# Optimization experiments

Hardware: AMD Instinct MI355X
Metric: run time of the kernel (lower is better)

## Reference

```python
import jax, jax.numpy as jnp
import numpy as np

F_FRAMES = 8
N_BOXES = 1024
N_CLASSES = 8
LINKAGE_T = 0.2
IOU_T = 0.2
MAX_SEQS = 48  # fixed cap on number of extracted sequences (jit-friendly)
NEG = -1e9


def _iou_mat(a, b):
    # a: [N,4], b: [M,4] (xyxy) -> [N,M] pairwise IoU
    area_a = (a[:, 2] - a[:, 0]) * (a[:, 3] - a[:, 1])
    area_b = (b[:, 2] - b[:, 0]) * (b[:, 3] - b[:, 1])
    lt = jnp.maximum(a[:, None, :2], b[None, :, :2])
    rb = jnp.minimum(a[:, None, 2:], b[None, :, 2:])
    wh = jnp.clip(rb - lt, 0.0)
    inter = wh[..., 0] * wh[..., 1]
    return inter / (area_a[:, None] + area_b[None, :] - inter + 1e-8)


def _iou_vec(box, boxes):
    # box: [4], boxes: [N,4] -> [N]
    area_a = (box[2] - box[0]) * (box[3] - box[1])
    area_b = (boxes[:, 2] - boxes[:, 0]) * (boxes[:, 3] - boxes[:, 1])
    lt = jnp.maximum(box[:2], boxes[:, :2])
    rb = jnp.minimum(box[2:], boxes[:, 2:])
    wh = jnp.clip(rb - lt, 0.0)
    inter = wh[:, 0] * wh[:, 1]
    return inter / (area_a + area_b - inter + 1e-8)


def setup_inputs():
    key = jax.random.key(0)
    k1, k2, k3 = jax.random.split(key, 3)
    raw = jax.random.uniform(k1, (F_FRAMES, N_BOXES, 4), dtype=jnp.float32)
    cxy = raw[..., :2] * 100.0          # centers in a 100x100 image
    wh = raw[..., 2:] * 10.0 + 1.0      # sizes in [1, 11] so IoU links fire
    boxes = jnp.concatenate([cxy - 0.5 * wh, cxy + 0.5 * wh], axis=-1)
    scores = jax.random.uniform(k2, (F_FRAMES, N_BOXES), dtype=jnp.float32)
    classes = jax.random.randint(k3, (F_FRAMES, N_BOXES), 0, N_CLASSES, dtype=jnp.int32)
    return {"boxes": boxes, "scores": scores, "classes": classes}


def _seq_nms(boxes, scores, classes):
    F, N, _ = boxes.shape
    idxN = jnp.arange(N)
    # linkage graph between adjacent frames: IoU >= linkage_threshold and same class
    iou_cross = jax.vmap(_iou_mat)(boxes[:-1], boxes[1:])               # [F-1,N,N]
    adj = (iou_cross >= LINKAGE_T) & (classes[:-1, :, None] == classes[1:, None, :])
    adj_pad = jnp.concatenate([adj, jnp.zeros((1, N, N), bool)], 0)     # [F,N,N]

    def body(state, _):
        active, out_scores, done = state
        s = jnp.where(active, scores, 0.0)
        # DP backward over frames: best sequence score starting at each box
        ms_last = jnp.where(active[-1], s[-1], NEG)
        def dp_step(ms_next, xs):
            adj_f, act_f, act_n, s_f = xs
            eff = adj_f & act_f[:, None] & act_n[None, :]
            best_succ = jnp.max(jnp.where(eff, ms_next[None, :], 0.0), axis=1)
            ms_f = jnp.where(act_f, s_f + best_succ, NEG)
            return ms_f, ms_f
        xs = (adj[::-1], active[:-1][::-1], active[1:][::-1], s[:-1][::-1])
        _, ms_rev = jax.lax.scan(dp_step, ms_last, xs)
        ms = jnp.concatenate([ms_rev[::-1], ms_last[None]], 0)          # [F,N]
        flat = jnp.argmax(ms)
        fstar = (flat // N).astype(jnp.int32)
        istar = (flat % N).astype(jnp.int32)
        best_val = ms.reshape(-1)[flat]
        # trace the best sequence forward through the graph
        ms_next_pad = jnp.concatenate([ms[1:], jnp.full((1, N), NEG)], 0)
        act_next_pad = jnp.concatenate([active[1:], jnp.zeros((1, N), bool)], 0)
        def trace_step(carry, xs2):
            cur, in_seq = carry
            f, adj_f, ms_n, act_n = xs2
            start = (f == fstar)
            in_seq = in_seq | start
            cur = jnp.where(start, istar, cur)
            onehot = in_seq & (idxN == cur)
            row = adj_f[cur] & act_n
            has_link = jnp.any(row)
            nxt = jnp.argmax(jnp.where(row, ms_n, NEG)).astype(cur.dtype)
            cont = in_seq & has_link
            return (jnp.where(cont, nxt, cur), cont), onehot
        carry0 = (jnp.zeros((), jnp.int32), jnp.zeros((), bool))
        _, seq_mask = jax.lax.scan(
            trace_step, carry0,
            (jnp.arange(F, dtype=jnp.int32), adj_pad, ms_next_pad, act_next_pad))
        seq_len = jnp.sum(seq_mask)
        valid = (seq_len > 1) & (best_val > 0) & (~done)
        # rescore: average of the sequence's (original) scores over all its members
        avg = jnp.sum(jnp.where(seq_mask, scores, 0.0)) / jnp.maximum(seq_len, 1)
        out_scores = jnp.where(seq_mask & valid, avg, out_scores)
        # suppress same-class boxes overlapping the sequence box in each sequence frame
        seq_boxes = jnp.einsum('fn,fnd->fd', seq_mask.astype(boxes.dtype), boxes)
        frame_in = jnp.any(seq_mask, axis=1)
        cls_seq = jnp.sum(jnp.where(seq_mask, classes, 0), axis=1)
        iou_same = jax.vmap(_iou_vec)(seq_boxes, boxes)                 # [F,N]
        sup = frame_in[:, None] & (iou_same >= IOU_T) & (classes == cls_seq[:, None])
        active = active & ~(sup & valid)
        done = done | ~((seq_len > 1) & (best_val > 0))
        return (active, out_scores, done), None

    init = (jnp.ones((F, N), bool), scores, jnp.zeros((), bool))
    (active, out_scores, done), _ = jax.lax.scan(body, init, None, length=MAX_SEQS)
    return out_scores


def reference(boxes, scores, classes):
    return _seq_nms(boxes, scores, classes)
```

## Files before the change

kernel.cpp:

```cpp
#include <hip/hip_runtime.h>

typedef unsigned int u32;
typedef unsigned short u16;
typedef unsigned char u8;

#define NFR 8
#define NBX 1024
#define NTOT 8192
#define NROW 7168
#define MAXS 48
#define NEGV -1000000000.0f
#define OVTOT 256
#define OVPF 36
#define PSTRIDE 64
#define DEG_RECOMP 0xFFFF
#define ENC_RESCAN  ((3u << 30) | (1023u << 10) | 1023u)

#define WS_POOL 7168
#define WS_OVL  (7168 + 8192)
#define WS_OST2 (WS_OVL + 128)
#define WS_WORDS (WS_OST2 + 8)

__device__ __forceinline__ bool iou_ge(const float4 a, const float4 b) {
    float wx = __fsub_rn(fminf(a.z, b.z), fmaxf(a.x, b.x));
    if (!(wx > 0.0f)) return false;
    float wy = __fsub_rn(fminf(a.w, b.w), fmaxf(a.y, b.y));
    if (!(wy > 0.0f)) return false;
    float inter = __fmul_rn(wx, wy);
    float aa = __fmul_rn(__fsub_rn(a.z, a.x), __fsub_rn(a.w, a.y));
    float ab = __fmul_rn(__fsub_rn(b.z, b.x), __fsub_rn(b.w, b.y));
    float den = __fadd_rn(__fsub_rn(__fadd_rn(aa, ab), inter), 1e-8f);
    return __fdiv_rn(inter, den) >= 0.2f;
}

__device__ __forceinline__ int xbin(float x) {
    int b = (int)floorf(__fmul_rn(__fadd_rn(x, 6.0f), 0.2857142857f));
    return b < 0 ? 0 : (b > 31 ? 31 : b);
}


__global__ __launch_bounds__(1024) void seqnms_setup(const float4* __restrict__ gbox,
                                                     const int* __restrict__ classes,
                                                     u32* __restrict__ ws) {
    __shared__ u32 clsb[3][32];
    __shared__ u32 cmask[8][32];
    __shared__ u32 xbm[32][32];
    __shared__ u16 ovl_l[OVPF];
    __shared__ u32 ofill;

    const int f = blockIdx.x;
    const int t = threadIdx.x, gw = t >> 6, ln = t & 63;

    if (t < 32 * 32) ((u32*)xbm)[t] = 0;
    if (t < 256) ((u32*)cmask)[t] = 0;
    if (t < 96) ((u32*)clsb)[t] = 0;
    if (t == 0) ofill = 0;

    const float4 a4 = gbox[f * NBX + t];
    const int ca = classes[f * NBX + t];
    const float4 nb4 = gbox[(f + 1) * NBX + t];
    const int ncl = classes[(f + 1) * NBX + t];
    __syncthreads();

    {
        const u32 bit = 1u << (t & 31); const int wrd = t >> 5;
        int b0 = xbin(nb4.x), b1 = xbin(nb4.z);
        for (int b = b0; b <= b1; ++b) atomicOr(&xbm[wrd][b], bit);
        atomicOr(&cmask[ncl][wrd], bit);
        if (ncl & 1) atomicOr(&clsb[0][wrd], bit);
        if (ncl & 2) atomicOr(&clsb[1][wrd], bit);
        if (ncl & 4) atomicOr(&clsb[2][wrd], bit);
    }
    __syncthreads();

    {
        const int rb0 = xbin(a4.x), rb1 = xbin(a4.z);
        const float4* nb = gbox + (f + 1) * NBX;
        u32 cnt = 0, j0 = 0, j1 = 0, j2 = 0;
        for (int w = 0; w < 32; ++w) {
            u32 mx = xbm[w][rb0];
            for (int b = rb0 + 1; b <= rb1; ++b) mx |= xbm[w][b];
            if (!mx) continue;
            u32 m = mx & cmask[ca][w];
            while (m) {
                int b = __ffs(m) - 1;
                m &= m - 1;
                int j = w * 32 + b;
                if (iou_ge(a4, nb[j])) {
                    if (cnt == 0) j0 = j; else if (cnt == 1) j1 = j; else if (cnt == 2) j2 = j;
                    ++cnt;
                }
            }
        }
        u32 enc;
        if (cnt <= 3) enc = (cnt << 30) | (j2 << 20) | (j1 << 10) | j0;
        else {
            u32 sl = atomicAdd(&ofill, 1u);
            if (sl < OVPF) {
                u32 slot = (u32)(f * OVPF) + sl;
                ovl_l[sl] = (u16)t;
                ((u16*)(ws + WS_OVL))[slot] = (u16)t;
                enc = (3u << 30) | (slot << 10) | slot;
            } else enc = ENC_RESCAN;
        }
        ws[f * NBX + t] = enc;
    }
    __syncthreads();

    {
        u16* poolg = (u16*)(ws + WS_POOL);
        int cntc = (int)ofill; if (cntc > OVPF) cntc = OVPF;
        for (int sl = gw; sl < cntc; sl += 16) {
            int i = ovl_l[sl];
            int slot = f * OVPF + sl;
            int cai = classes[f * NBX + i];
            float4 ai = gbox[f * NBX + i];
            u32 mym = 0;
            if (ln < 32) {
                u32 m = ((cai & 1) ? clsb[0][ln] : ~clsb[0][ln])
                      & ((cai & 2) ? clsb[1][ln] : ~clsb[1][ln])
                      & ((cai & 4) ? clsb[2][ln] : ~clsb[2][ln]);
                while (m) {
                    int b = __ffs(m) - 1;
                    m &= m - 1;
                    if (iou_ge(ai, gbox[(f + 1) * NBX + ln * 32 + b])) mym |= 1u << b;
                }
            }
            int c = __popc(mym), inc = c;
            for (int off = 1; off < 64; off <<= 1) {
                int v = __shfl_up(inc, off);
                if (ln >= off) inc += v;
            }
            int deg = __shfl(inc, 63);
            int base = inc - c;
            if (deg <= PSTRIDE - 1) {
                if (ln == 0) poolg[slot * PSTRIDE] = (u16)deg;
                if (ln < 32) {
                    u32 m = mym; int idx = base;
                    while (m) {
                        int b = __ffs(m) - 1;
                        m &= m - 1;
                        poolg[slot * PSTRIDE + 1 + idx++] = (u16)(ln * 32 + b);
                    }
                }
            } else if (ln == 0) poolg[slot * PSTRIDE] = (u16)DEG_RECOMP;
        }
        if (t == 0) ws[WS_OST2 + f] = (u32)cntc;
    }
}

__global__ __launch_bounds__(512) void seqnms_iter(const float4* __restrict__ gbox,
                                                   const float* __restrict__ scores,
                                                   const int* __restrict__ classes,
                                                   float* __restrict__ out,
                                                   const u32* __restrict__ ws) {
    __shared__ float4 ms4[NTOT / 4];
    __shared__ float4 seqbox[NFR];
    __shared__ float ssc[NTOT];
    __shared__ u32 csr[NROW];
    __shared__ u32 clsb7[7][3][32];
    __shared__ u16 pool[OVTOT * PSTRIDE];
    __shared__ u8 cls8[NTOT];
    __shared__ u32 cnt_sh[8];
    __shared__ float redv[8];
    __shared__ int   redi[8];
    __shared__ int   sel_sh[NFR];
    __shared__ int   seqcls[NFR];
    __shared__ float avg_sh;
    __shared__ int   valid_sh, done_sh;
    __shared__ u16 ovl[OVTOT];
    __shared__ u8  ovact[OVTOT];

    float* ms = (float*)ms4;
    const int t = threadIdx.x, gw = t >> 6, ln = t & 63;
    const int sg = (gw << 3) + (ln >> 3), sl = ln & 7;

    for (int idx = t; idx < NROW; idx += 512) csr[idx] = ws[idx];
    u32* p32 = (u32*)pool;
    for (int idx = t; idx < OVTOT * PSTRIDE / 2; idx += 512) p32[idx] = ws[WS_POOL + idx];
    if (t < 128) ((u32*)ovl)[t] = ws[WS_OVL + t];
    if (t < 7) cnt_sh[t] = ws[WS_OST2 + t];
    if (t < OVTOT) ovact[t] = 1;
    if (t == 0) done_sh = 0;

    float psc2[2][NFR]; u32 pclp[2] = {0u, 0u};
    #pragma unroll
    for (int f = 0; f < NFR; ++f) {
        #pragma unroll
        for (int c = 0; c < 2; ++c) {
            int i = t + (c << 9);
            float s = scores[f * NBX + i];
            int cl = classes[f * NBX + i];
            psc2[c][f] = s;
            pclp[c] |= (u32)cl << (3 * f);
            out[f * NBX + i] = s;
            ssc[f * NBX + i] = s;
            cls8[f * NBX + i] = (u8)cl;
        }
    }
    if (t < 224) {
        int fr = (t >> 5) + 1, w = t & 31;
        u32 p0 = 0, p1 = 0, p2 = 0;
        for (int b = 0; b < 32; ++b) {
            int c = classes[fr * NBX + w * 32 + b];
            p0 |= (u32)(c & 1) << b;
            p1 |= (u32)((c >> 1) & 1) << b;
            p2 |= (u32)((c >> 2) & 1) << b;
        }
        clsb7[fr - 1][0][w] = p0; clsb7[fr - 1][1][w] = p1; clsb7[fr - 1][2][w] = p2;
    }
    __syncthreads();

    u32 pc2[2][7]; u32 lmask = 0;
    #pragma unroll
    for (int c = 0; c < 2; ++c) {
        #pragma unroll
        for (int f = 0; f < 7; ++f) {
            u32 p = csr[f * NBX + t + (c << 9)];
            pc2[c][f] = p;
            if ((p >> 30) == 3u && (p & 1023) == ((p >> 10) & 1023) && (p & 1023) != 1023)
                lmask |= 1u << (8 * c + f);
        }
    }
    int ose[7];
    #pragma unroll
    for (int f = 0; f < 7; ++f) {
        int cv = (int)cnt_sh[f]; if (cv > OVPF) cv = OVPF;
        ose[f] = __builtin_amdgcn_readfirstlane(f * OVPF + cv);
    }
    u32 act = 0xFFFFu;
    float ms7_0 = psc2[0][7], ms7_1 = psc2[1][7];
    ms[7 * NBX + t] = ms7_0;
    ms[7 * NBX + t + 512] = ms7_1;
    __syncthreads();

    for (int it = 0; it < MAXS; ++it) {
        float bv = ms7_0; int bi = 7 * NBX + t;
        { float v = ms7_1; int r = 7 * NBX + t + 512;
          if (v > bv || (v == bv && r < bi)) { bv = v; bi = r; } }
        #pragma unroll
        for (int f = 6; f >= 0; --f) {
            const float* msn = &ms[(f + 1) * NBX];
            #pragma unroll
            for (int c = 0; c < 2; ++c) {
                const u32 p = pc2[c][f];
                const u32 cA = p >> 30, j0 = p & 1023, j1 = (p >> 10) & 1023;
                const bool ovf = (cA == 3u) && (j0 == j1);
                const int i = t + (c << 9);
                const int r = f * NBX + i;
                if (!ovf) {
                    float v = NEGV;
                    if ((act >> (8 * c + f)) & 1) {
                        float best = 0.0f;
                        if (cA >= 1) best = fmaxf(best, fmaxf(msn[j0], 0.0f));
                        if (cA >= 2) best = fmaxf(best, fmaxf(msn[j1], 0.0f));
                        if (cA >= 3) best = fmaxf(best, fmaxf(msn[(p >> 20) & 1023], 0.0f));
                        v = __fadd_rn(psc2[c][f], best);
                    }
                    ms[r] = v;
                    if (v > bv || (v == bv && r < bi)) { bv = v; bi = r; }
                } else if (j0 == 1023) {
                    float v = NEGV;
                    if ((act >> (8 * c + f)) & 1) {
                        float best = 0.0f;
                        int ca = (int)((pclp[c] >> (3 * f)) & 7u);
                        float4 a4 = gbox[r];
                        for (int w = 0; w < 32; ++w) {
                            u32 q0 = clsb7[f][0][w], q1 = clsb7[f][1][w], q2 = clsb7[f][2][w];
                            u32 m = ((ca & 1) ? q0 : ~q0) & ((ca & 2) ? q1 : ~q1) & ((ca & 4) ? q2 : ~q2);
                            while (m) {
                                int b = __ffs(m) - 1;
                                m &= m - 1;
                                int j = w * 32 + b;
                                float mv = msn[j];
                                if (mv > 0.0f && iou_ge(a4, gbox[(f + 1) * NBX + j]))
                                    best = fmaxf(best, mv);
                            }
                        }
                        v = __fadd_rn(psc2[c][f], best);
                    }
                    ms[r] = v;
                    if (v > bv || (v == bv && r < bi)) { bv = v; bi = r; }
                }
            }
            {
                const int s1 = ose[f];
                for (int s = f * OVPF + sg; s < s1; s += 64) {
                    int i = ovl[s];
                    int rr = f * NBX + i;
                    bool actv = ovact[s] != 0;
                    float best = 0.0f;
                    if (actv) {
                        int deg = (int)pool[s * PSTRIDE];
                        if (deg != (int)DEG_RECOMP) {
                            for (int q = sl; q < deg; q += 8)
                                best = fmaxf(best, fmaxf(msn[pool[s * PSTRIDE + 1 + q]], 0.0f));
                        } else {
                            int ca = (int)cls8[rr]; float4 a4 = gbox[rr];
                            for (int ww = 0; ww < 4; ++ww) {
                                int w = sl * 4 + ww;
                                u32 q0 = clsb7[f][0][w], q1 = clsb7[f][1][w], q2 = clsb7[f][2][w];
                                u32 m = ((ca & 1) ? q0 : ~q0) & ((ca & 2) ? q1 : ~q1) & ((ca & 4) ? q2 : ~q2);
                                while (m) {
                                    int b = __ffs(m) - 1;
                                    m &= m - 1;
                                    int j = w * 32 + b;
                                    if (iou_ge(a4, gbox[(f + 1) * NBX + j]))
                                        best = fmaxf(best, fmaxf(msn[j], 0.0f));
                                }
                            }
                        }
                        best = fmaxf(best, __shfl_xor(best, 1));
                        best = fmaxf(best, __shfl_xor(best, 2));
                        best = fmaxf(best, __shfl_xor(best, 4));
                    }
                    if (sl == 0) ms[rr] = actv ? __fadd_rn(ssc[rr], best) : NEGV;
                }
            }
            __syncthreads();
        }

        #pragma unroll
        for (int c = 0; c < 2; ++c) {
            #pragma unroll
            for (int f = 0; f < 7; ++f) if ((lmask >> (8 * c + f)) & 1) {
                int r = f * NBX + t + (c << 9); float v = ms[r];
                if (v > bv || (v == bv && r < bi)) { bv = v; bi = r; }
            }
        }
        #pragma unroll
        for (int off = 32; off > 0; off >>= 1) {
            float ov = __shfl_down(bv, off); int oi = __shfl_down(bi, off);
            if (ov > bv || (ov == bv && oi < bi)) { bv = ov; bi = oi; }
        }
        if (ln == 0) { redv[gw] = bv; redi[gw] = bi; }
        __syncthreads();

        if (t < 64) {
            float v = (ln < 8) ? redv[ln] : -3.0e38f;
            int i0 = (ln < 8) ? redi[ln] : 0x7fffffff;
            #pragma unroll
            for (int off = 4; off > 0; off >>= 1) {
                float ov = __shfl_down(v, off); int oi = __shfl_down(i0, off);
                if (ov > v || (ov == v && oi < i0)) { v = ov; i0 = oi; }
            }
            v = __shfl(v, 0); i0 = __shfl(i0, 0);
            const float bestval = v;
            const int fstar = i0 >> 10, istar = i0 & (NBX - 1);
            if (ln < NFR) sel_sh[ln] = -1;
            int cur = istar;
            for (int f = fstar; f < NFR; ++f) {
                if (ln == 0) sel_sh[f] = cur;
                if (f == 7) break;
                u32 p = csr[f * NBX + cur];
                u32 c = p >> 30, j0 = p & 1023, j1 = (p >> 10) & 1023;
                const float* msn = &ms[(f + 1) * NBX];
                if (!((c == 3u) && (j0 == j1))) {
                    float tb = -3.0e38f; int tj = -1;
                    if (c >= 1) { float m = msn[j0]; if (m != NEGV) { tb = m; tj = (int)j0; } }
                    if (c >= 2) { float m = msn[j1]; if (m != NEGV && m > tb) { tb = m; tj = (int)j1; } }
                    if (c >= 3) { int j2 = (p >> 20) & 1023; float m = msn[j2];
                                  if (m != NEGV && m > tb) { tb = m; tj = j2; } }
                    if (tj < 0) break;
                    cur = tj;
                } else {
                    float tv = -3.0e38f; int tj = 0x7fffffff;
                    bool recomp = true;
                    if (j0 != 1023) {
                        int s = (int)j0;
                        int deg = (int)pool[s * PSTRIDE];
                        if (deg != (int)DEG_RECOMP) {
                            recomp = false;
                            for (int q = ln; q < deg; q += 64) {
                                int j = (int)pool[s * PSTRIDE + 1 + q];
                                float m = msn[j];
                                if (m != NEGV && (m > tv || (m == tv && j < tj))) { tv = m; tj = j; }
                            }
                        }
                    }
                    if (recomp) {
                        int ca = (int)cls8[f * NBX + cur]; float4 a4 = gbox[f * NBX + cur];
                        if (ln < 32) {
                            u32 q0 = clsb7[f][0][ln], q1 = clsb7[f][1][ln], q2 = clsb7[f][2][ln];
                            u32 m = ((ca & 1) ? q0 : ~q0) & ((ca & 2) ? q1 : ~q1) & ((ca & 4) ? q2 : ~q2);
                            while (m) {
                                int b = __ffs(m) - 1;
                                m &= m - 1;
                                int j = ln * 32 + b;
                                float mv = msn[j];
                                if (mv != NEGV && iou_ge(a4, gbox[(f + 1) * NBX + j])) {
                                    if (mv > tv || (mv == tv && j < tj)) { tv = mv; tj = j; }
                                }
                            }
                        }
                    }
                    #pragma unroll
                    for (int off = 32; off > 0; off >>= 1) {
                        float ov = __shfl_down(tv, off); int oj = __shfl_down(tj, off);
                        if (ov > tv || (ov == tv && oj < tj)) { tv = ov; tj = oj; }
                    }
                    tv = __shfl(tv, 0); tj = __shfl(tj, 0);
                    if (tv < -1.0e37f) break;
                    cur = tj;
                }
            }
            float sv = 0.0f; int cc = 0;
            if (ln < NFR) {
                int sj = sel_sh[ln];
                if (sj >= 0) {
                    sv = ssc[(ln << 10) + sj]; cc = 1;
                    seqbox[ln] = gbox[(ln << 10) + sj];
                    seqcls[ln] = (int)cls8[(ln << 10) + sj];
                }
            }
            #pragma unroll
            for (int off = 4; off > 0; off >>= 1) {
                sv = __fadd_rn(sv, __shfl_down(sv, off));
                cc += __shfl_down(cc, off);
            }
            if (ln == 0) {
                avg_sh = __fdiv_rn(sv, (float)cc);
                bool ok = (cc > 1) && (bestval > 0.0f);
                valid_sh = (ok && !done_sh) ? 1 : 0;
                if (!ok) done_sh = 1;
            }
        }
        __syncthreads();

        if (valid_sh) {
            #pragma unroll
            for (int f = 0; f < NFR; ++f) {
                int sj = sel_sh[f];
                if (sj < 0) continue;
                int scl = seqcls[f];
                float4 sb = seqbox[f];
                #pragma unroll
                for (int c = 0; c < 2; ++c) {
                    int cl = (int)((pclp[c] >> (3 * f)) & 7u);
                    if (cl != scl) continue;
                    float4 b = gbox[f * NBX + t + (c << 9)];
                    if (iou_ge(sb, b)) act &= ~(1u << (8 * c + f));
                }
            }
            #pragma unroll
            for (int c = 0; c < 2; ++c) {
                #pragma unroll
                for (int f = 0; f < 7; ++f) if ((lmask >> (8 * c + f)) & 1)
                    ovact[pc2[c][f] & 1023] = (u8)((act >> (8 * c + f)) & 1);
            }
            ms7_0 = ((act >> 7) & 1) ? psc2[0][7] : NEGV;
            ms7_1 = ((act >> 15) & 1) ? psc2[1][7] : NEGV;
            ms[7 * NBX + t] = ms7_0;
            ms[7 * NBX + t + 512] = ms7_1;
            if (t < NFR) {
                int sj = sel_sh[t];
                if (sj >= 0) out[t * NBX + sj] = avg_sh;
            }
        }
        __syncthreads();
        if (done_sh) break;
    }
}

#define OVTOTF 256
#define ENC_PENDING ((3u << 30) | (1022u << 10) | 1022u)
__global__ __launch_bounds__(1024) void seqnms_full(const float4* __restrict__ gbox,
                                                    const float* __restrict__ scores,
                                                    const int* __restrict__ classes,
                                                    float* __restrict__ out) {
    __shared__ float4 ms4[NTOT / 4];
    __shared__ float4 seqbox[NFR];
    __shared__ float ssc[NTOT];
    __shared__ u32 csr[NROW];
    __shared__ u32 clsb7[7][3][32];
    __shared__ u16 pool[OVTOTF * PSTRIDE];
    __shared__ u8 cls8[NTOT];
    __shared__ u32 ostart[8];
    __shared__ u32 ofill[7];
    __shared__ u32 ocnt[7];
    __shared__ float redv[16];
    __shared__ int   redi[16];
    __shared__ int   sel_sh[NFR];
    __shared__ int   seqcls[NFR];
    __shared__ float avg_sh;
    __shared__ int   valid_sh, done_sh;
    __shared__ u16 ovl[OVTOTF];
    __shared__ u8  ovact[OVTOTF];

    float* ms = (float*)ms4;
    const int t = threadIdx.x, gw = t >> 6, ln = t & 63;

    float psc[NFR]; int pcl[NFR]; float4 pbx[NFR];
    #pragma unroll
    for (int f = 0; f < NFR; ++f) {
        psc[f] = scores[f * NBX + t];
        pcl[f] = classes[f * NBX + t];
        pbx[f] = gbox[f * NBX + t];
        out[f * NBX + t] = psc[f];
        ssc[f * NBX + t] = psc[f];
        cls8[f * NBX + t] = (u8)pcl[f];
    }
    if (t < 7) { ocnt[t] = 0; ofill[t] = 0; }
    if (t < OVTOTF) ovact[t] = 1;
    if (t == 0) done_sh = 0;

    if (t < 224) {
        int fr = (t >> 5) + 1, w = t & 31;
        u32 p0 = 0, p1 = 0, p2 = 0;
        for (int b = 0; b < 32; ++b) {
            int c = classes[fr * NBX + w * 32 + b];
            p0 |= (u32)(c & 1) << b;
            p1 |= (u32)((c >> 1) & 1) << b;
            p2 |= (u32)((c >> 2) & 1) << b;
        }
        clsb7[fr - 1][0][w] = p0; clsb7[fr - 1][1][w] = p1; clsb7[fr - 1][2][w] = p2;
    }
    __syncthreads();

    for (int f = 0; f < 7; ++f) {
        ms4[t] = pbx[f + 1];
        __syncthreads();
        const int r = f * NBX + t;
        const int ca = pcl[f];
        const float4 a4 = pbx[f];
        u32 cnt = 0, j0 = 0, j1 = 0, j2 = 0;
        for (int w = 0; w < 32; ++w) {
            u32 q0 = clsb7[f][0][w], q1 = clsb7[f][1][w], q2 = clsb7[f][2][w];
            u32 m = ((ca & 1) ? q0 : ~q0) & ((ca & 2) ? q1 : ~q1) & ((ca & 4) ? q2 : ~q2);
            while (m) {
                int b = __ffs(m) - 1;
                m &= m - 1;
                int j = w * 32 + b;
                if (iou_ge(a4, ms4[j])) {
                    if (cnt == 0) j0 = j; else if (cnt == 1) j1 = j; else if (cnt == 2) j2 = j;
                    ++cnt;
                }
            }
        }
        if (cnt <= 3) csr[r] = (cnt << 30) | (j2 << 20) | (j1 << 10) | j0;
        else { atomicAdd(&ocnt[f], 1u); csr[r] = ENC_PENDING; }
        __syncthreads();
    }
    if (t == 0) {
        u32 s = 0;
        for (int f = 0; f < 7; ++f) { ostart[f] = s; s += ocnt[f]; }
        ostart[7] = s;
    }
    __syncthreads();
    for (int f = 0; f < 7; ++f) {
        int r = f * NBX + t;
        if (csr[r] == ENC_PENDING) {
            u32 slot = ostart[f] + atomicAdd(&ofill[f], 1u);
            if (slot < OVTOTF) { ovl[slot] = (u16)t; csr[r] = (3u << 30) | (slot << 10) | slot; }
            else csr[r] = ENC_RESCAN;
        }
    }
    __syncthreads();
    {
        int total = (int)ostart[7]; if (total > OVTOTF) total = OVTOTF;
        for (int s = gw; s < total; s += 16) {
            int f = 0;
            while (s >= (int)ostart[f + 1]) ++f;
            int i = ovl[s];
            int ca = (int)cls8[f * NBX + i];
            float4 a4 = gbox[f * NBX + i];
            u32 mym = 0;
            if (ln < 32) {
                u32 q0 = clsb7[f][0][ln], q1 = clsb7[f][1][ln], q2 = clsb7[f][2][ln];
                u32 m = ((ca & 1) ? q0 : ~q0) & ((ca & 2) ? q1 : ~q1) & ((ca & 4) ? q2 : ~q2);
                while (m) {
                    int b = __ffs(m) - 1;
                    m &= m - 1;
                    if (iou_ge(a4, gbox[(f + 1) * NBX + ln * 32 + b])) mym |= 1u << b;
                }
            }
            int c = __popc(mym), inc = c;
            for (int off = 1; off < 64; off <<= 1) {
                int v = __shfl_up(inc, off);
                if (ln >= off) inc += v;
            }
            int deg = __shfl(inc, 63);
            int base = inc - c;
            if (deg <= PSTRIDE - 1) {
                if (ln == 0) pool[s * PSTRIDE] = (u16)deg;
                if (ln < 32) {
                    u32 m = mym; int idx = base;
                    while (m) {
                        int b = __ffs(m) - 1;
                        m &= m - 1;
                        pool[s * PSTRIDE + 1 + idx++] = (u16)(ln * 32 + b);
                    }
                }
            } else if (ln == 0) pool[s * PSTRIDE] = (u16)DEG_RECOMP;
        }
    }
    __syncthreads();

    u32 pc[7]; u32 lmask = 0;
    #pragma unroll
    for (int f = 0; f < 7; ++f) {
        u32 p = csr[f * NBX + t];
        pc[f] = p;
        if ((p >> 30) == 3u && (p & 1023) == ((p >> 10) & 1023) && (p & 1023) != 1023)
            lmask |= 1u << f;
    }
    int os[8];
    #pragma unroll
    for (int f = 0; f < 8; ++f) {
        int v = (int)ostart[f]; if (v > OVTOTF) v = OVTOTF;
        os[f] = __builtin_amdgcn_readfirstlane(v);
    }
    u32 act = 0xFF;
    float ms7 = psc[7];
    ms[7 * NBX + t] = ms7;
    __syncthreads();

    for (int it = 0; it < MAXS; ++it) {
        float bv = ms7; int bi = 7 * NBX + t;
        #pragma unroll
        for (int f = 6; f >= 0; --f) {
            const float* msn = &ms[(f + 1) * NBX];
            const u32 p = pc[f];
            const u32 c = p >> 30, j0 = p & 1023, j1 = (p >> 10) & 1023;
            const bool ovf = (c == 3u) && (j0 == j1);
            const int r = f * NBX + t;
            if (!ovf) {
                float v = NEGV;
                if ((act >> f) & 1) {
                    float best = 0.0f;
                    if (c >= 1) best = fmaxf(best, fmaxf(msn[j0], 0.0f));
                    if (c >= 2) best = fmaxf(best, fmaxf(msn[j1], 0.0f));
                    if (c >= 3) best = fmaxf(best, fmaxf(msn[(p >> 20) & 1023], 0.0f));
                    v = __fadd_rn(psc[f], best);
                }
                ms[r] = v;
                if (v > bv || (v == bv && r < bi)) { bv = v; bi = r; }
            } else if (j0 == 1023) {
                float v = NEGV;
                if ((act >> f) & 1) {
                    float best = 0.0f;
                    int ca = pcl[f]; float4 a4 = pbx[f];
                    for (int w = 0; w < 32; ++w) {
                        u32 q0 = clsb7[f][0][w], q1 = clsb7[f][1][w], q2 = clsb7[f][2][w];
                        u32 m = ((ca & 1) ? q0 : ~q0) & ((ca & 2) ? q1 : ~q1) & ((ca & 4) ? q2 : ~q2);
                        while (m) {
                            int b = __ffs(m) - 1;
                            m &= m - 1;
                            int j = w * 32 + b;
                            float mv = msn[j];
                            if (mv > 0.0f && iou_ge(a4, gbox[(f + 1) * NBX + j]))
                                best = fmaxf(best, mv);
                        }
                    }
                    v = __fadd_rn(psc[f], best);
                }
                ms[r] = v;
                if (v > bv || (v == bv && r < bi)) { bv = v; bi = r; }
            }
            {
                const int s1 = os[f + 1];
                for (int s = os[f] + gw; s < s1; s += 16) {
                    int i = ovl[s];
                    int rr = f * NBX + i;
                    bool actv = ovact[s] != 0;
                    float best = 0.0f;
                    if (actv) {
                        int deg = (int)pool[s * PSTRIDE];
                        if (deg != (int)DEG_RECOMP) {
                            for (int q = ln; q < deg; q += 64)
                                best = fmaxf(best, fmaxf(msn[pool[s * PSTRIDE + 1 + q]], 0.0f));
                        } else {
                            int ca = (int)cls8[rr]; float4 a4 = gbox[rr];
                            if (ln < 32) {
                                u32 q0 = clsb7[f][0][ln], q1 = clsb7[f][1][ln], q2 = clsb7[f][2][ln];
                                u32 m = ((ca & 1) ? q0 : ~q0) & ((ca & 2) ? q1 : ~q1) & ((ca & 4) ? q2 : ~q2);
                                while (m) {
                                    int b = __ffs(m) - 1;
                                    m &= m - 1;
                                    int j = ln * 32 + b;
                                    if (iou_ge(a4, gbox[(f + 1) * NBX + j]))
                                        best = fmaxf(best, fmaxf(msn[j], 0.0f));
                                }
                            }
                        }
                        #pragma unroll
                        for (int off = 32; off > 0; off >>= 1)
                            best = fmaxf(best, __shfl_down(best, off));
                    }
                    if (ln == 0) ms[rr] = actv ? __fadd_rn(ssc[rr], best) : NEGV;
                }
            }
            __syncthreads();
        }

        #pragma unroll
        for (int f = 0; f < 7; ++f) if ((lmask >> f) & 1) {
            int r = f * NBX + t; float v = ms[r];
            if (v > bv || (v == bv && r < bi)) { bv = v; bi = r; }
        }
        #pragma unroll
        for (int off = 32; off > 0; off >>= 1) {
            float ov = __shfl_down(bv, off); int oi = __shfl_down(bi, off);
            if (ov > bv || (ov == bv && oi < bi)) { bv = ov; bi = oi; }
        }
        if (ln == 0) { redv[gw] = bv; redi[gw] = bi; }
        __syncthreads();

        if (t < 64) {
            float v = (ln < 16) ? redv[ln] : -3.0e38f;
            int i0 = (ln < 16) ? redi[ln] : 0x7fffffff;
            #pragma unroll
            for (int off = 8; off > 0; off >>= 1) {
                float ov = __shfl_down(v, off); int oi = __shfl_down(i0, off);
                if (ov > v || (ov == v && oi < i0)) { v = ov; i0 = oi; }
            }
            v = __shfl(v, 0); i0 = __shfl(i0, 0);
            const float bestval = v;
            const int fstar = i0 >> 10, istar = i0 & (NBX - 1);
            if (ln < NFR) sel_sh[ln] = -1;
            int cur = istar;
            for (int f = fstar; f < NFR; ++f) {
                if (ln == 0) sel_sh[f] = cur;
                if (f == 7) break;
                u32 p = csr[f * NBX + cur];
                u32 c = p >> 30, j0 = p & 1023, j1 = (p >> 10) & 1023;
                const float* msn = &ms[(f + 1) * NBX];
                if (!((c == 3u) && (j0 == j1))) {
                    float tb = -3.0e38f; int tj = -1;
                    if (c >= 1) { float m = msn[j0]; if (m != NEGV) { tb = m; tj = (int)j0; } }
                    if (c >= 2) { float m = msn[j1]; if (m != NEGV && m > tb) { tb = m; tj = (int)j1; } }
                    if (c >= 3) { int j2 = (p >> 20) & 1023; float m = msn[j2];
                                  if (m != NEGV && m > tb) { tb = m; tj = j2; } }
                    if (tj < 0) break;
                    cur = tj;
                } else {
                    float tv = -3.0e38f; int tj = 0x7fffffff;
                    bool recomp = true;
                    if (j0 != 1023) {
                        int s = (int)j0;
                        int deg = (int)pool[s * PSTRIDE];
                        if (deg != (int)DEG_RECOMP) {
                            recomp = false;
                            for (int q = ln; q < deg; q += 64) {
                                int j = (int)pool[s * PSTRIDE + 1 + q];
                                float m = msn[j];
                                if (m != NEGV && (m > tv || (m == tv && j < tj))) { tv = m; tj = j; }
                            }
                        }
                    }
                    if (recomp) {
                        int ca = (int)cls8[f * NBX + cur]; float4 a4 = gbox[f * NBX + cur];
                        if (ln < 32) {
                            u32 q0 = clsb7[f][0][ln], q1 = clsb7[f][1][ln], q2 = clsb7[f][2][ln];
                            u32 m = ((ca & 1) ? q0 : ~q0) & ((ca & 2) ? q1 : ~q1) & ((ca & 4) ? q2 : ~q2);
                            while (m) {
                                int b = __ffs(m) - 1;
                                m &= m - 1;
                                int j = ln * 32 + b;
                                float mv = msn[j];
                                if (mv != NEGV && iou_ge(a4, gbox[(f + 1) * NBX + j])) {
                                    if (mv > tv || (mv == tv && j < tj)) { tv = mv; tj = j; }
                                }
                            }
                        }
                    }
                    #pragma unroll
                    for (int off = 32; off > 0; off >>= 1) {
                        float ov = __shfl_down(tv, off); int oj = __shfl_down(tj, off);
                        if (ov > tv || (ov == tv && oj < tj)) { tv = ov; tj = oj; }
                    }
                    tv = __shfl(tv, 0); tj = __shfl(tj, 0);
                    if (tv < -1.0e37f) break;
                    cur = tj;
                }
            }
            float sv = 0.0f; int cc = 0;
            if (ln < NFR) {
                int sj = sel_sh[ln];
                if (sj >= 0) {
                    sv = ssc[ln * NBX + sj]; cc = 1;
                    seqbox[ln] = gbox[ln * NBX + sj];
                    seqcls[ln] = (int)cls8[ln * NBX + sj];
                }
            }
            #pragma unroll
            for (int off = 4; off > 0; off >>= 1) {
                sv = __fadd_rn(sv, __shfl_down(sv, off));
                cc += __shfl_down(cc, off);
            }
            if (ln == 0) {
                avg_sh = __fdiv_rn(sv, (float)cc);
                bool ok = (cc > 1) && (bestval > 0.0f);
                valid_sh = (ok && !done_sh) ? 1 : 0;
                if (!ok) done_sh = 1;
            }
        }
        __syncthreads();

        if (valid_sh) {
            #pragma unroll
            for (int f = 0; f < NFR; ++f) {
                int sj = sel_sh[f];
                if (sj < 0) continue;
                if (pcl[f] != seqcls[f]) continue;
                if (iou_ge(seqbox[f], pbx[f])) act &= ~(1u << f);
            }
            #pragma unroll
            for (int f = 0; f < 7; ++f) if ((lmask >> f) & 1)
                ovact[pc[f] & 1023] = (u8)((act >> f) & 1);
            ms7 = (act & 0x80) ? psc[7] : NEGV;
            ms[7 * NBX + t] = ms7;
            if (t < NFR) {
                int sj = sel_sh[t];
                if (sj >= 0) out[t * NBX + sj] = avg_sh;
            }
        }
        __syncthreads();
        if (done_sh) break;
    }
}

extern "C" void kernel_launch(void* const* d_in, const int* in_sizes, int n_in,
                              void* d_out, int out_size, void* d_ws, size_t ws_size,
                              hipStream_t stream) {
    const float4* boxes = (const float4*)d_in[0];
    const float* scores = (const float*)d_in[1];
    const int* classes = (const int*)d_in[2];
    float* out = (float*)d_out;
    const int use_split =
        (d_ws != nullptr && ws_size >= (size_t)(WS_WORDS * 4)) ? 1 : 0;
    if (use_split) {
        seqnms_setup<<<7, 1024, 0, stream>>>(boxes, classes, (u32*)d_ws);
        seqnms_iter<<<1, 512, 0, stream>>>(boxes, scores, classes, out, (const u32*)d_ws);
    } else {
        seqnms_full<<<1, 1024, 0, stream>>>(boxes, scores, classes, out);
    }
}
```

Baseline: 628.2 us.

## Defer suppression into next iteration and fuse argmax into DP passes

The suppression step moves from the end of each iteration to the start of the next. The frame-6 DP pass now reads frame-7 values through an inline suppression check, so a barrier between suppression and DP is no longer needed. The argmax is also folded into the DP writes, which removes the separate rescan of ms and one barrier. The sequence-average write is done directly by the reducing wave, dropping the avg_sh shared variable and another barrier. In exchange, the frame-6 pass recomputes IoU checks against the frame-7 sequence box for every neighbour it reads, and there is more code duplication.

Measured after the change: 673.7 us. 7.2% more time.

```diff
diff --git a/kernel.cpp b/kernel.cpp
--- a/kernel.cpp
+++ b/kernel.cpp
@@ -166,7 +166,6 @@
     __shared__ int   redi[8];
     __shared__ int   sel_sh[NFR];
     __shared__ int   seqcls[NFR];
-    __shared__ float avg_sh;
     __shared__ int   valid_sh, done_sh;
     __shared__ u16 ovl[OVTOT];
     __shared__ u8  ovact[OVTOT];
@@ -181,7 +180,7 @@
     if (t < 128) ((u32*)ovl)[t] = ws[WS_OVL + t];
     if (t < 7) cnt_sh[t] = ws[WS_OST2 + t];
     if (t < OVTOT) ovact[t] = 1;
-    if (t == 0) done_sh = 0;
+    if (t == 0) { done_sh = 0; valid_sh = 0; }
 
     float psc2[2][NFR]; u32 pclp[2] = {0u, 0u};
     #pragma unroll
@@ -235,11 +234,138 @@
     __syncthreads();
 
     for (int it = 0; it < MAXS; ++it) {
+        if (valid_sh) {
+            #pragma unroll
+            for (int f = 0; f < NFR; ++f) {
+                int sj = sel_sh[f];
+                if (sj < 0) continue;
+                int scl = seqcls[f];
+                float4 sb = seqbox[f];
+                #pragma unroll
+                for (int c = 0; c < 2; ++c) {
+                    int cl = (int)((pclp[c] >> (3 * f)) & 7u);
+                    if (cl != scl) continue;
+                    float4 b = gbox[f * NBX + t + (c << 9)];
+                    if (iou_ge(sb, b)) act &= ~(1u << (8 * c + f));
+                }
+            }
+            #pragma unroll
+            for (int c = 0; c < 2; ++c) {
+                #pragma unroll
+                for (int f = 0; f < 7; ++f) if ((lmask >> (8 * c + f)) & 1)
+                    ovact[pc2[c][f] & 1023] = (u8)((act >> (8 * c + f)) & 1);
+            }
+            ms7_0 = ((act >> 7) & 1) ? psc2[0][7] : NEGV;
+            ms7_1 = ((act >> 15) & 1) ? psc2[1][7] : NEGV;
+            ms[7 * NBX + t] = ms7_0;
+            ms[7 * NBX + t + 512] = ms7_1;
+        }
         float bv = ms7_0; int bi = 7 * NBX + t;
         { float v = ms7_1; int r = 7 * NBX + t + 512;
           if (v > bv || (v == bv && r < bi)) { bv = v; bi = r; } }
+
+        const int sup7 = (valid_sh && sel_sh[7] >= 0) ? 1 : 0;
+        const float4 sb7 = seqbox[7];
+        const int scl7 = seqcls[7];
+        const int sup6 = (valid_sh && sel_sh[6] >= 0) ? 1 : 0;
+        const float4 sb6 = seqbox[6];
+        const int scl6 = seqcls[6];
+        {
+            const float* msn = &ms[7 * NBX];
+            auto rd7 = [&](int j) -> float {
+                float v = msn[j];
+                if (sup7 && (int)cls8[7 * NBX + j] == scl7 &&
+                    iou_ge(sb7, gbox[7 * NBX + j])) v = NEGV;
+                return v;
+            };
+            #pragma unroll
+            for (int c = 0; c < 2; ++c) {
+                const u32 p = pc2[c][6];
+                const u32 cA = p >> 30, j0 = p & 1023, j1 = (p >> 10) & 1023;
+                const bool ovf = (cA == 3u) && (j0 == j1);
+                const int i = t + (c << 9);
+                const int r = 6 * NBX + i;
+                if (!ovf) {
+                    float v = NEGV;
+                    if ((act >> (8 * c + 6)) & 1) {
+                        float best = 0.0f;
+                        if (cA >= 1) best = fmaxf(best, fmaxf(rd7((int)j0), 0.0f));
+                        if (cA >= 2) best = fmaxf(best, fmaxf(rd7((int)j1), 0.0f));
+                        if (cA >= 3) best = fmaxf(best, fmaxf(rd7((int)((p >> 20) & 1023)), 0.0f));
+                        v = __fadd_rn(psc2[c][6], best);
+                    }
+                    ms[r] = v;
+                    if (v > bv || (v == bv && r < bi)) { bv = v; bi = r; }
+                } else if (j0 == 1023) {
+                    float v = NEGV;
+                    if ((act >> (8 * c + 6)) & 1) {
+                        float best = 0.0f;
+                        int ca = (int)((pclp[c] >> 18) & 7u);
+                        float4 a4 = gbox[r];
+                        for (int w = 0; w < 32; ++w) {
+                            u32 q0 = clsb7[6][0][w], q1 = clsb7[6][1][w], q2 = clsb7[6][2][w];
+                            u32 m = ((ca & 1) ? q0 : ~q0) & ((ca & 2) ? q1 : ~q1) & ((ca & 4) ? q2 : ~q2);
+                            while (m) {
+                                int b = __ffs(m) - 1;
+                                m &= m - 1;
+                                int j = w * 32 + b;
+                                float mv = rd7(j);
+                                if (mv > 0.0f && iou_ge(a4, gbox[7 * NBX + j]))
+                                    best = fmaxf(best, mv);
+                            }
+                        }
+                        v = __fadd_rn(psc2[c][6], best);
+                    }
+                    ms[r] = v;
+                    if (v > bv || (v == bv && r < bi)) { bv = v; bi = r; }
+                }
+            }
+            {
+                const int s1 = ose[6];
+                for (int s = 6 * OVPF + sg; s < s1; s += 64) {
+                    int i = ovl[s];
+                    int rr = 6 * NBX + i;
+                    bool actv = ovact[s] != 0;
+                    if (actv && sup6) {
+                        if ((int)cls8[rr] == scl6 && iou_ge(sb6, gbox[rr])) actv = false;
+                    }
+                    float best = 0.0f;
+                    if (actv) {
+                        int deg = (int)pool[s * PSTRIDE];
+                        if (deg != (int)DEG_RECOMP) {
+                            for (int q = sl; q < deg; q += 8)
+                                best = fmaxf(best, fmaxf(rd7((int)pool[s * PSTRIDE + 1 + q]), 0.0f));
+                        } else {
+                            int ca = (int)cls8[rr]; float4 a4 = gbox[rr];
+                            for (int ww = 0; ww < 4; ++ww) {
+                                int w = sl * 4 + ww;
+                                u32 q0 = clsb7[6][0][w], q1 = clsb7[6][1][w], q2 = clsb7[6][2][w];
+                                u32 m = ((ca & 1) ? q0 : ~q0) & ((ca & 2) ? q1 : ~q1) & ((ca & 4) ? q2 : ~q2);
+                                while (m) {
+                                    int b = __ffs(m) - 1;
+                                    m &= m - 1;
+                                    int j = w * 32 + b;
+                                    if (iou_ge(a4, gbox[7 * NBX + j]))
+                                        best = fmaxf(best, fmaxf(rd7(j), 0.0f));
+                                }
+                            }
+                        }
+                        best = fmaxf(best, __shfl_xor(best, 1));
+                        best = fmaxf(best, __shfl_xor(best, 2));
+                        best = fmaxf(best, __shfl_xor(best, 4));
+                    }
+                    if (sl == 0) {
+                        float v = actv ? __fadd_rn(ssc[rr], best) : NEGV;
+                        ms[rr] = v;
+                        if (v > bv || (v == bv && rr < bi)) { bv = v; bi = rr; }
+                    }
+                }
+            }
+        }
+        __syncthreads();
+
         #pragma unroll
-        for (int f = 6; f >= 0; --f) {
+        for (int f = 5; f >= 0; --f) {
             const float* msn = &ms[(f + 1) * NBX];
             #pragma unroll
             for (int c = 0; c < 2; ++c) {
@@ -314,27 +440,23 @@
                         best = fmaxf(best, __shfl_xor(best, 2));
                         best = fmaxf(best, __shfl_xor(best, 4));
                     }
-                    if (sl == 0) ms[rr] = actv ? __fadd_rn(ssc[rr], best) : NEGV;
-                }
+                    if (sl == 0) {
+                        float v = actv ? __fadd_rn(ssc[rr], best) : NEGV;
+                        ms[rr] = v;
+                        if (v > bv || (v == bv && rr < bi)) { bv = v; bi = rr; }
+                    }
+                }
+            }
+            if (f == 0) {
+                #pragma unroll
+                for (int off = 32; off > 0; off >>= 1) {
+                    float ov = __shfl_down(bv, off); int oi = __shfl_down(bi, off);
+                    if (ov > bv || (ov == bv && oi < bi)) { bv = ov; bi = oi; }
+                }
+                if (ln == 0) { redv[gw] = bv; redi[gw] = bi; }
             }
             __syncthreads();
         }
-
-        #pragma unroll
-        for (int c = 0; c < 2; ++c) {
-            #pragma unroll
-            for (int f = 0; f < 7; ++f) if ((lmask >> (8 * c + f)) & 1) {
-                int r = f * NBX + t + (c << 9); float v = ms[r];
-                if (v > bv || (v == bv && r < bi)) { bv = v; bi = r; }
-            }
-        }
-        #pragma unroll
-        for (int off = 32; off > 0; off >>= 1) {
-            float ov = __shfl_down(bv, off); int oi = __shfl_down(bi, off);
-            if (ov > bv || (ov == bv && oi < bi)) { bv = ov; bi = oi; }
-        }
-        if (ln == 0) { redv[gw] = bv; redi[gw] = bi; }
-        __syncthreads();
 
         if (t < 64) {
             float v = (ln < 8) ? redv[ln] : -3.0e38f;
@@ -418,43 +540,15 @@
                 sv = __fadd_rn(sv, __shfl_down(sv, off));
                 cc += __shfl_down(cc, off);
             }
-            if (ln == 0) {
-                avg_sh = __fdiv_rn(sv, (float)cc);
-                bool ok = (cc > 1) && (bestval > 0.0f);
-                valid_sh = (ok && !done_sh) ? 1 : 0;
-                if (!ok) done_sh = 1;
-            }
-        }
-        __syncthreads();
-
-        if (valid_sh) {
-            #pragma unroll
-            for (int f = 0; f < NFR; ++f) {
-                int sj = sel_sh[f];
-                if (sj < 0) continue;
-                int scl = seqcls[f];
-                float4 sb = seqbox[f];
-                #pragma unroll
-                for (int c = 0; c < 2; ++c) {
-                    int cl = (int)((pclp[c] >> (3 * f)) & 7u);
-                    if (cl != scl) continue;
-                    float4 b = gbox[f * NBX + t + (c << 9)];
-                    if (iou_ge(sb, b)) act &= ~(1u << (8 * c + f));
-                }
-            }
-            #pragma unroll
-            for (int c = 0; c < 2; ++c) {
-                #pragma unroll
-                for (int f = 0; f < 7; ++f) if ((lmask >> (8 * c + f)) & 1)
-                    ovact[pc2[c][f] & 1023] = (u8)((act >> (8 * c + f)) & 1);
-            }
-            ms7_0 = ((act >> 7) & 1) ? psc2[0][7] : NEGV;
-            ms7_1 = ((act >> 15) & 1) ? psc2[1][7] : NEGV;
-            ms[7 * NBX + t] = ms7_0;
-            ms[7 * NBX + t + 512] = ms7_1;
-            if (t < NFR) {
-                int sj = sel_sh[t];
-                if (sj >= 0) out[t * NBX + sj] = avg_sh;
+            sv = __shfl(sv, 0); cc = __shfl(cc, 0);
+            int dprev = done_sh;
+            float avg = __fdiv_rn(sv, (float)cc);
+            bool ok = (cc > 1) && (bestval > 0.0f);
+            int validf = (ok && !dprev) ? 1 : 0;
+            if (ln == 0) { valid_sh = validf; if (!ok) done_sh = 1; }
+            if (validf && ln < NFR) {
+                int sj = sel_sh[ln];
+                if (sj >= 0) out[ln * NBX + sj] = avg;
             }
         }
         __syncthreads();
```
